# Optimization experiments

Hardware: AMD Instinct MI355X
Metric: run time of the kernel (lower is better)

The kernel has to match this reference:

```python
import jax, jax.numpy as jnp
import numpy as np

N_NODES = 50000


def setup_inputs() -> dict:
    key = jax.random.key(0)
    ks = jax.random.split(key, 5)
    d_in, d_out = 96, 96
    x = jax.random.normal(ks[0], (N_NODES, d_in), dtype=jnp.float32)
    edge_index = jax.random.randint(ks[1], (2, 800000), 0, N_NODES, dtype=jnp.int64)
    W_gcn = jax.random.normal(ks[2], (d_in, d_out), dtype=jnp.float32) / np.sqrt(d_in)
    b_gcn = jnp.zeros((d_out,), dtype=jnp.float32)
    W_lin = jax.random.normal(ks[3], (d_in, d_out), dtype=jnp.float32) / np.sqrt(d_in)
    b_lin = jnp.zeros((d_out,), dtype=jnp.float32)
    return {"x": x, "edge_index": edge_index, "W_gcn": W_gcn, "b_gcn": b_gcn,
            "W_lin": W_lin, "b_lin": b_lin}


def mish(y):
    return y * jnp.tanh(jax.nn.softplus(y))


def gcn_conv(x, edge_index, W, b):
    n = x.shape[0]
    # add self-loops (PyG GCNConv default)
    loop = jnp.arange(n, dtype=edge_index.dtype)
    src = jnp.concatenate([edge_index[0], loop])  # [E+N]
    dst = jnp.concatenate([edge_index[1], loop])
    h = x @ W  # [N, d_out]
    # symmetric normalization: deg over destination nodes of A+I
    deg = jax.ops.segment_sum(jnp.ones_like(dst, dtype=h.dtype), dst, num_segments=n)
    dinv = jnp.where(deg > 0, jax.lax.rsqrt(deg), 0.0)
    norm = dinv[src] * dinv[dst]  # [E+N]
    msg = h[src] * norm[:, None]  # gather + scale
    agg = jax.ops.segment_sum(msg, dst, num_segments=n)  # scatter-add
    return agg + b


def reference(x, edge_index, W_gcn, b_gcn, W_lin, b_lin):
    x_gcn = gcn_conv(x, edge_index, W_gcn, b_gcn)
    x_skip = x @ W_lin + b_lin
    return mish(x_gcn + x_skip)
```

## Files before the change

kernel.cpp:

```cpp
#include <hip/hip_runtime.h>
#include <hip/hip_bf16.h>
#include <math.h>

#define D 96
#define CAP 48
#define NXCD 8
#define FILL_GPB 160

typedef __attribute__((ext_vector_type(8))) short bf16x8;
typedef __attribute__((ext_vector_type(4))) float f32x4;
typedef __attribute__((ext_vector_type(8))) unsigned short u16x8;

__global__ __launch_bounds__(256) void prep_kernel(const float* __restrict__ Wg,
                                                   const float* __restrict__ Wl,
                                                   __hip_bfloat16* __restrict__ wT,
                                                   int* __restrict__ cursor, int n) {
    int i = blockIdx.x * 256 + threadIdx.x;
    if (i < n) cursor[i] = 0;
    if (i < 192 * D) {
        int c = i / D, k = i % D;
        float v = (c < D) ? Wg[k * D + c] : Wl[k * D + (c - D)];
        wT[i] = __float2bfloat16(v);
    }
}

__global__ __launch_bounds__(256) void fill_bucket_kernel(
    const int* __restrict__ src, const int* __restrict__ dst,
    int* __restrict__ cursor, unsigned short* __restrict__ bucket,
    int e, int n)
{
    int g = blockIdx.x & (NXCD - 1);
    int bc = blockIdx.x >> 3;
    int lo = (g * n) / NXCD;
    int hi = ((g + 1) * n) / NXCD;
    int stride = FILL_GPB * 256;
#pragma unroll 4
    for (int i = bc * 256 + threadIdx.x; i < e; i += stride) {
        int d = __builtin_nontemporal_load(&dst[i]);
        if (d >= lo && d < hi) {
            int s = __builtin_nontemporal_load(&src[i]);
            int pos = atomicAdd(&cursor[d], 1);
            if (pos < CAP) bucket[(size_t)d * CAP + pos] = (unsigned short)s;
        }
    }
}

__global__ __launch_bounds__(256) void gemm_mfma_kernel(
    const float* __restrict__ x, const __hip_bfloat16* __restrict__ wT,
    const float* __restrict__ bl, const int* __restrict__ cursor,
    __hip_bfloat16* __restrict__ hp, float* __restrict__ out, int n)
{
    __shared__ __hip_bfloat16 sw[192 * D];
    int tid = threadIdx.x;
    int rbase = blockIdx.x * 64;

    {
        const ushort4* s4 = (const ushort4*)wT;
        ushort4* d4 = (ushort4*)sw;
        for (int i = tid; i < 192 * D / 4; i += 256) d4[i] = s4[i];
    }

    int w = tid >> 6, l = tid & 63;
    int lrow = l & 15, lk = (l >> 4) * 8;
    int arow = rbase + w * 16 + lrow;

    bf16x8 a[3];
    if (arow < n) {
        const float* xr = &x[(size_t)arow * D];
#pragma unroll
        for (int kc = 0; kc < 3; kc++) {
            float4 u = *(const float4*)&xr[kc * 32 + lk];
            float4 v = *(const float4*)&xr[kc * 32 + lk + 4];
            __hip_bfloat16 t[8];
            t[0] = __float2bfloat16(u.x); t[1] = __float2bfloat16(u.y);
            t[2] = __float2bfloat16(u.z); t[3] = __float2bfloat16(u.w);
            t[4] = __float2bfloat16(v.x); t[5] = __float2bfloat16(v.y);
            t[6] = __float2bfloat16(v.z); t[7] = __float2bfloat16(v.w);
            a[kc] = *(const bf16x8*)t;
        }
    } else {
#pragma unroll
        for (int kc = 0; kc < 3; kc++) a[kc] = (bf16x8){0,0,0,0,0,0,0,0};
    }
    __syncthreads();

    f32x4 acc[12];
#pragma unroll
    for (int ct = 0; ct < 12; ct++) acc[ct] = (f32x4){0.f, 0.f, 0.f, 0.f};

#pragma unroll
    for (int ct = 0; ct < 12; ct++) {
#pragma unroll
        for (int kc = 0; kc < 3; kc++) {
            bf16x8 b = *(const bf16x8*)&sw[(ct * 16 + lrow) * D + kc * 32 + lk];
            acc[ct] = __builtin_amdgcn_mfma_f32_16x16x32_bf16(a[kc], b, acc[ct], 0, 0, 0);
        }
    }

    int col0 = l & 15;
#pragma unroll
    for (int j = 0; j < 4; j++) {
        int row = rbase + w * 16 + (l >> 4) * 4 + j;
        if (row < n) {
            float dinv = rsqrtf((float)(cursor[row] + 1));
            size_t hb = (size_t)row * D;
#pragma unroll
            for (int ct = 0; ct < 6; ct++)
                hp[hb + ct * 16 + col0] = __float2bfloat16(acc[ct][j] * dinv);
#pragma unroll
            for (int ct = 0; ct < 6; ct++) {
                int c = ct * 16 + col0;
                out[hb + c] = acc[6 + ct][j] + bl[c];
            }
        }
    }
}

__device__ __forceinline__ float mish_f(float v) {
    float u = __expf(v);
    float t = u * u + 2.f * u;
    float m = v * t / (t + 2.f);
    return (v > 30.f) ? v : m;
}

__global__ __launch_bounds__(256) void gather_kernel(
    const __hip_bfloat16* __restrict__ hp, const int* __restrict__ cursor,
    const unsigned short* __restrict__ bucket, const float* __restrict__ bg,
    float* __restrict__ out, int n)
{
    __shared__ unsigned short sbk[8 * CAP];
    __shared__ int sdeg[8];
    int tid = threadIdx.x;
    int nb0 = blockIdx.x * 8;

    int navail = n - nb0; if (navail > 8) navail = 8;
    int nu32 = navail * (CAP / 2);
    if (tid < nu32)
        ((unsigned int*)sbk)[tid] =
            ((const unsigned int*)(bucket + (size_t)nb0 * CAP))[tid];
    if (tid < navail) sdeg[tid] = cursor[nb0 + tid];
    __syncthreads();

    int g = tid >> 5;
    int lane = tid & 31;
    int sub = lane >> 4;
    int j = lane & 15;
    bool active = (j < 12);
    int d = nb0 + g;
    if (d >= n) return;

    int deg = sdeg[g];
    int cnt = deg < CAP ? deg : CAP;
    const unsigned short* bk = &sbk[g * CAP];
    const unsigned short* hpu = (const unsigned short*)hp;

    float a0[8], a1[8];
#pragma unroll
    for (int k = 0; k < 8; k++) { a0[k] = 0.f; a1[k] = 0.f; }

    if (sub == 0 && active) {
        u16x8 v = *(const u16x8*)&hpu[(size_t)d * D + j * 8];
#pragma unroll
        for (int k = 0; k < 8; k++)
            a0[k] += __uint_as_float(((unsigned int)v[k]) << 16);
    }

    for (int e = sub; e < cnt; e += 16) {
        u16x8 v[8];
#pragma unroll
        for (int i = 0; i < 8; i++) {
            int ee = e + 2 * i;
            if (ee < cnt && active)
                v[i] = *(const u16x8*)&hpu[(size_t)bk[ee] * D + j * 8];
        }
#pragma unroll
        for (int i = 0; i < 8; i++) {
            int ee = e + 2 * i;
            if (ee < cnt && active) {
                float* ac = (i & 1) ? a1 : a0;
#pragma unroll
                for (int k = 0; k < 8; k++)
                    ac[k] += __uint_as_float(((unsigned int)v[i][k]) << 16);
            }
        }
    }

#pragma unroll
    for (int k = 0; k < 8; k++) a0[k] += a1[k];
#pragma unroll
    for (int k = 0; k < 8; k++) a0[k] += __shfl_xor(a0[k], 16, 32);

    if (sub == 0 && active) {
        float dinv = rsqrtf((float)(deg + 1));
        size_t ob = (size_t)d * D + j * 8;
        float4 s0 = *(const float4*)&out[ob];
        float4 s1 = *(const float4*)&out[ob + 4];
        float4 b0 = *(const float4*)&bg[j * 8];
        float4 b1 = *(const float4*)&bg[j * 8 + 4];
        float r[8];
        r[0] = mish_f(a0[0] * dinv + b0.x + s0.x);
        r[1] = mish_f(a0[1] * dinv + b0.y + s0.y);
        r[2] = mish_f(a0[2] * dinv + b0.z + s0.z);
        r[3] = mish_f(a0[3] * dinv + b0.w + s0.w);
        r[4] = mish_f(a0[4] * dinv + b1.x + s1.x);
        r[5] = mish_f(a0[5] * dinv + b1.y + s1.y);
        r[6] = mish_f(a0[6] * dinv + b1.z + s1.z);
        r[7] = mish_f(a0[7] * dinv + b1.w + s1.w);
        *(float4*)&out[ob]     = make_float4(r[0], r[1], r[2], r[3]);
        *(float4*)&out[ob + 4] = make_float4(r[4], r[5], r[6], r[7]);
    }
}

extern "C" void kernel_launch(void* const* d_in, const int* in_sizes, int n_in,
                              void* d_out, int out_size, void* d_ws, size_t ws_size,
                              hipStream_t stream)
{
    const float* x  = (const float*)d_in[0];
    const int* edge = (const int*)d_in[1];
    const float* Wg = (const float*)d_in[2];
    const float* bg = (const float*)d_in[3];
    const float* Wl = (const float*)d_in[4];
    const float* bl = (const float*)d_in[5];
    float* out = (float*)d_out;

    const int n = in_sizes[0] / D;
    const int e = in_sizes[1] / 2;
    const int* src = edge;
    const int* dst = edge + e;

    int* cursor = (int*)d_ws;
    size_t off_b = ((size_t)n * sizeof(int) + 255) & ~(size_t)255;
    __hip_bfloat16* wT = (__hip_bfloat16*)((char*)d_ws + off_b);
    off_b += (size_t)192 * D * sizeof(__hip_bfloat16);
    off_b = (off_b + 255) & ~(size_t)255;
    __hip_bfloat16* hp = (__hip_bfloat16*)((char*)d_ws + off_b);
    off_b += (size_t)n * D * sizeof(__hip_bfloat16);
    off_b = (off_b + 255) & ~(size_t)255;
    unsigned short* bucket = (unsigned short*)((char*)d_ws + off_b);

    int prep_blocks = (n + 255) / 256;
    prep_kernel<<<prep_blocks, 256, 0, stream>>>(Wg, Wl, wT, cursor, n);
    fill_bucket_kernel<<<NXCD * FILL_GPB, 256, 0, stream>>>(src, dst, cursor, bucket, e, n);
    gemm_mfma_kernel<<<(n + 63) / 64, 256, 0, stream>>>(x, wT, bl, cursor, hp, out, n);
    gather_kernel<<<(n + 7) / 8, 256, 0, stream>>>(hp, cursor, bucket, bg, out, n);
}
```

Baseline: 167.7 us.

## Drop XCD-partitioned bucket fill, add nontemporal loads/stores, deepen gather batch

The bucket-fill kernel no longer partitions destination ranges by XCD. It now uses one thread per edge with a plain atomic slot claim and a nontemporal store. Nontemporal loads and stores are added for the x reads, the skip-output writes, the bucket loads and the final output in the gather kernel. The gather loop issues 12 outstanding row loads per pass instead of 8. This trades the per-XCD L2 locality of cursor atomics for less redundant reading of the edge list, and risks more cross-XCD atomic traffic and higher register pressure.

```diff
diff --git a/kernel.cpp b/kernel.cpp
--- a/kernel.cpp
+++ b/kernel.cpp
@@ -4,8 +4,6 @@
 
 #define D 96
 #define CAP 48
-#define NXCD 8
-#define FILL_GPB 160
 
 typedef __attribute__((ext_vector_type(8))) short bf16x8;
 typedef __attribute__((ext_vector_type(4))) float f32x4;
@@ -26,22 +24,16 @@
 
 __global__ __launch_bounds__(256) void fill_bucket_kernel(
     const int* __restrict__ src, const int* __restrict__ dst,
-    int* __restrict__ cursor, unsigned short* __restrict__ bucket,
-    int e, int n)
-{
-    int g = blockIdx.x & (NXCD - 1);
-    int bc = blockIdx.x >> 3;
-    int lo = (g * n) / NXCD;
-    int hi = ((g + 1) * n) / NXCD;
-    int stride = FILL_GPB * 256;
-#pragma unroll 4
-    for (int i = bc * 256 + threadIdx.x; i < e; i += stride) {
+    int* __restrict__ cursor, unsigned short* __restrict__ bucket, int e)
+{
+    int i = blockIdx.x * 256 + threadIdx.x;
+    if (i < e) {
         int d = __builtin_nontemporal_load(&dst[i]);
-        if (d >= lo && d < hi) {
-            int s = __builtin_nontemporal_load(&src[i]);
-            int pos = atomicAdd(&cursor[d], 1);
-            if (pos < CAP) bucket[(size_t)d * CAP + pos] = (unsigned short)s;
-        }
+        int s = __builtin_nontemporal_load(&src[i]);
+        int pos = atomicAdd(&cursor[d], 1);
+        if (pos < CAP)
+            __builtin_nontemporal_store((unsigned short)s,
+                                        &bucket[(size_t)d * CAP + pos]);
     }
 }
 
@@ -69,8 +61,8 @@
         const float* xr = &x[(size_t)arow * D];
 #pragma unroll
         for (int kc = 0; kc < 3; kc++) {
-            float4 u = *(const float4*)&xr[kc * 32 + lk];
-            float4 v = *(const float4*)&xr[kc * 32 + lk + 4];
+            f32x4 u = __builtin_nontemporal_load((const f32x4*)&xr[kc * 32 + lk]);
+            f32x4 v = __builtin_nontemporal_load((const f32x4*)&xr[kc * 32 + lk + 4]);
             __hip_bfloat16 t[8];
             t[0] = __float2bfloat16(u.x); t[1] = __float2bfloat16(u.y);
             t[2] = __float2bfloat16(u.z); t[3] = __float2bfloat16(u.w);
@@ -110,7 +102,7 @@
 #pragma unroll
             for (int ct = 0; ct < 6; ct++) {
                 int c = ct * 16 + col0;
-                out[hb + c] = acc[6 + ct][j] + bl[c];
+                __builtin_nontemporal_store(acc[6 + ct][j] + bl[c], &out[hb + c]);
             }
         }
     }
@@ -136,8 +128,8 @@
     int navail = n - nb0; if (navail > 8) navail = 8;
     int nu32 = navail * (CAP / 2);
     if (tid < nu32)
-        ((unsigned int*)sbk)[tid] =
-            ((const unsigned int*)(bucket + (size_t)nb0 * CAP))[tid];
+        ((unsigned int*)sbk)[tid] = __builtin_nontemporal_load(
+            (const unsigned int*)(bucket + (size_t)nb0 * CAP) + tid);
     if (tid < navail) sdeg[tid] = cursor[nb0 + tid];
     __syncthreads();
 
@@ -165,16 +157,16 @@
             a0[k] += __uint_as_float(((unsigned int)v[k]) << 16);
     }
 
-    for (int e = sub; e < cnt; e += 16) {
-        u16x8 v[8];
-#pragma unroll
-        for (int i = 0; i < 8; i++) {
+    for (int e = sub; e < cnt; e += 24) {
+        u16x8 v[12];
+#pragma unroll
+        for (int i = 0; i < 12; i++) {
             int ee = e + 2 * i;
             if (ee < cnt && active)
                 v[i] = *(const u16x8*)&hpu[(size_t)bk[ee] * D + j * 8];
         }
 #pragma unroll
-        for (int i = 0; i < 8; i++) {
+        for (int i = 0; i < 12; i++) {
             int ee = e + 2 * i;
             if (ee < cnt && active) {
                 float* ac = (i & 1) ? a1 : a0;
@@ -193,21 +185,21 @@
     if (sub == 0 && active) {
         float dinv = rsqrtf((float)(deg + 1));
         size_t ob = (size_t)d * D + j * 8;
-        float4 s0 = *(const float4*)&out[ob];
-        float4 s1 = *(const float4*)&out[ob + 4];
-        float4 b0 = *(const float4*)&bg[j * 8];
-        float4 b1 = *(const float4*)&bg[j * 8 + 4];
-        float r[8];
-        r[0] = mish_f(a0[0] * dinv + b0.x + s0.x);
-        r[1] = mish_f(a0[1] * dinv + b0.y + s0.y);
-        r[2] = mish_f(a0[2] * dinv + b0.z + s0.z);
-        r[3] = mish_f(a0[3] * dinv + b0.w + s0.w);
-        r[4] = mish_f(a0[4] * dinv + b1.x + s1.x);
-        r[5] = mish_f(a0[5] * dinv + b1.y + s1.y);
-        r[6] = mish_f(a0[6] * dinv + b1.z + s1.z);
-        r[7] = mish_f(a0[7] * dinv + b1.w + s1.w);
-        *(float4*)&out[ob]     = make_float4(r[0], r[1], r[2], r[3]);
-        *(float4*)&out[ob + 4] = make_float4(r[4], r[5], r[6], r[7]);
+        f32x4 s0 = __builtin_nontemporal_load((const f32x4*)&out[ob]);
+        f32x4 s1 = __builtin_nontemporal_load((const f32x4*)&out[ob + 4]);
+        f32x4 b0 = *(const f32x4*)&bg[j * 8];
+        f32x4 b1 = *(const f32x4*)&bg[j * 8 + 4];
+        f32x4 r0, r1;
+        r0.x = mish_f(a0[0] * dinv + b0.x + s0.x);
+        r0.y = mish_f(a0[1] * dinv + b0.y + s0.y);
+        r0.z = mish_f(a0[2] * dinv + b0.z + s0.z);
+        r0.w = mish_f(a0[3] * dinv + b0.w + s0.w);
+        r1.x = mish_f(a0[4] * dinv + b1.x + s1.x);
+        r1.y = mish_f(a0[5] * dinv + b1.y + s1.y);
+        r1.z = mish_f(a0[6] * dinv + b1.z + s1.z);
+        r1.w = mish_f(a0[7] * dinv + b1.w + s1.w);
+        __builtin_nontemporal_store(r0, (f32x4*)&out[ob]);
+        __builtin_nontemporal_store(r1, (f32x4*)&out[ob + 4]);
     }
 }
 
@@ -240,7 +232,7 @@
 
     int prep_blocks = (n + 255) / 256;
     prep_kernel<<<prep_blocks, 256, 0, stream>>>(Wg, Wl, wT, cursor, n);
-    fill_bucket_kernel<<<NXCD * FILL_GPB, 256, 0, stream>>>(src, dst, cursor, bucket, e, n);
+    fill_bucket_kernel<<<(e + 255) / 256, 256, 0, stream>>>(src, dst, cursor, bucket, e);
     gemm_mfma_kernel<<<(n + 63) / 64, 256, 0, stream>>>(x, wT, bl, cursor, hp, out, n);
     gather_kernel<<<(n + 7) / 8, 256, 0, stream>>>(hp, cursor, bucket, bg, out, n);
 }
```

New measurement: 181.9 us. 8.5% more time.
